# Performance work log

Measured on AMD Instinct MI355X. Metric: run time of the kernel, lower is better.

Reference implementation:

```python
import jax, jax.numpy as jnp
import numpy as np

jax.config.update("jax_enable_x64", True)  # int64 keys for lattice hashing

_EPS = float(np.finfo(np.float64).eps)
_SIGMA_SPATIAL = 5.0   # spatial stddev (voxels)
_SIGMA_COLOR = 0.25    # intensity stddev
_BASE = 8192           # per-coordinate key range
_OFF = 4096            # coordinate offset so packed keys are non-negative


def _encode(coords):
    """Pack (..., d) integer lattice coords into a single int64 key."""
    enc = jnp.zeros(coords.shape[:-1], jnp.int64)
    for i in range(coords.shape[-1]):
        enc = enc * _BASE + (coords[..., i].astype(jnp.int64) + _OFF)
    return enc


def _bilateral_features(image):
    """Bilateral features: (z,y,x)/sigma_s and intensity/sigma_c. image: (1,D,H,W)."""
    _, D, H, W = image.shape
    z, y, x = jnp.meshgrid(jnp.arange(D, dtype=jnp.float32),
                           jnp.arange(H, dtype=jnp.float32),
                           jnp.arange(W, dtype=jnp.float32), indexing="ij")
    spatial = jnp.stack([z, y, x], -1) / _SIGMA_SPATIAL            # (D,H,W,3)
    color = (image[0] / _SIGMA_COLOR)[..., None]                   # (D,H,W,1)
    return jnp.concatenate([spatial, color], -1).reshape(-1, 4)    # (N,4)


def _permutohedral(q, feats):
    """Permutohedral-lattice Gaussian filtering (splat -> blur -> slice).
    q: (N,C) float32 values, feats: (N,d) float32 positions. Returns (N,C).
    Global scale of the blur kernel cancels in the final normalization."""
    N, d = feats.shape
    dp1 = d + 1
    # ---- elevate features onto the hyperplane H_d ----
    inv_std = np.sqrt(2.0 / 3.0) * dp1
    scale = jnp.asarray([inv_std / np.sqrt((i + 1) * (i + 2)) for i in range(d)], jnp.float32)
    cf = feats * scale
    elev = [None] * dp1
    sm = jnp.zeros((N,), jnp.float32)
    for i in range(d, 0, -1):
        c = cf[:, i - 1]
        elev[i] = sm - i * c
        sm = sm + c
    elev[0] = sm
    elevated = jnp.stack(elev, axis=1)                             # (N, d+1)
    # ---- closest remainder-0 lattice point ----
    rd = jnp.round(elevated / dp1)
    rem0 = rd * dp1
    sum_rd = jnp.sum(rd, axis=1).astype(jnp.int32)
    # ---- rank of each coordinate (ties broken by index) ----
    diff = elevated - rem0
    di = diff[:, :, None]
    dj = diff[:, None, :]
    jlt = (jnp.arange(dp1)[None, :] < jnp.arange(dp1)[:, None])[None]  # mask[i,j] = j < i
    rank = jnp.sum((dj > di) | ((dj == di) & jlt), axis=2).astype(jnp.int32)
    rank = rank + sum_rd[:, None]
    low, high = rank < 0, rank > d
    rank = rank + jnp.where(low, dp1, 0) - jnp.where(high, dp1, 0)
    rem0 = rem0 + jnp.where(low, float(dp1), 0.0) - jnp.where(high, float(dp1), 0.0)
    # ---- barycentric coordinates inside the enclosing simplex ----
    v = (elevated - rem0) / dp1
    rows = jnp.arange(N)[:, None]
    bary = jnp.zeros((N, d + 2), jnp.float32)
    bary = bary.at[rows, d - rank].add(v)
    bary = bary.at[rows, dp1 - rank].add(-v)
    bary = bary.at[:, 0].add(1.0 + bary[:, dp1])
    bary = bary[:, :dp1]                                           # (N, d+1) weights per remainder
    # ---- integer keys of the d+1 simplex vertices (first d coords suffice) ----
    rem0i = rem0[:, :d].astype(jnp.int32)
    keys = jnp.stack([rem0i + jnp.where(rank[:, :d] < dp1 - r, r, r - dp1).astype(jnp.int32)
                      for r in range(dp1)], axis=1)                # (N, d+1, d)
    enc = _encode(keys).reshape(-1)
    Mpad = N * dp1
    sentinel = _BASE ** d                                          # > any real key; sorts last
    uniq, inv = jnp.unique(enc, return_inverse=True, size=Mpad, fill_value=sentinel)
    inv = inv.reshape(N, dp1)
    # ---- splat ----
    C = q.shape[1]
    vals = jnp.zeros((Mpad, C), jnp.float32).at[inv].add(bary[:, :, None] * q[:, None, :])
    # ---- blur along each of the d+1 lattice directions ----
    coords = jnp.stack([(uniq // (_BASE ** (d - 1 - i))) % _BASE - _OFF for i in range(d)],
                       axis=-1).astype(jnp.int32)                  # (Mpad, d)

    def lookup(c):
        e = _encode(c)
        pos = jnp.clip(jnp.searchsorted(uniq, e), 0, Mpad - 1)
        return pos, uniq[pos] == e

    for j in range(dp1):
        off = jnp.ones((d,), jnp.int32)
        if j < d:
            off = off.at[j].set(-d)
        p1, f1 = lookup(coords + off)
        p2, f2 = lookup(coords - off)
        n1 = jnp.where(f1[:, None], vals[p1], 0.0)
        n2 = jnp.where(f2[:, None], vals[p2], 0.0)
        vals = 0.5 * vals + 0.25 * (n1 + n2)
    # ---- slice ----
    return jnp.sum(bary[:, :, None] * vals[inv], axis=1)           # (N, C)


def setup_inputs():
    key = jax.random.key(0)
    k1, k2 = jax.random.split(key)
    input_ = jax.random.uniform(k1, (4, 96, 96, 96), dtype=jnp.float32)
    image = jax.random.uniform(k2, (1, 96, 96, 96), dtype=jnp.float32)
    return {"input_": input_, "image": image}


def reference(input_, image):
    feats = _bilateral_features(image)
    C, D, H, W = input_.shape
    q = input_.reshape(C, -1).T                                    # (N, C)
    ones = jnp.ones((q.shape[0], 1), jnp.float32)                  # fused normalization pass
    filt = _permutohedral(jnp.concatenate([q, ones], axis=1), feats)
    out = filt[:, :C] / (filt[:, C:] + _EPS)                       # == permuto(q) * 1/(permuto(1)+eps)
    return out.T.reshape(C, D, H, W)
```

## Files before the change

kernel.cpp:

```cpp
#include <hip/hip_runtime.h>
#include <hip/hip_fp16.h>
#include <stdint.h>

#define NPTS (96*96*96)
#define NP5  (NPTS*5)

#define GD1 33
#define GD2 29
#define GD3 25
#define GO0 5
#define GO1 16
#define GO2 18
#define GO3 19
#define GS3 5
#define GS2 (GD3*GS3)
#define GS1 (GD2*GS2)
#define GS0 (GD1*GS1)
#define GCELLS (31*GS0)
#define GCELLS1 (GCELLS+1)
#define GSSUM (GS0+GS1+GS2+GS3)

#define LHS 2048

struct LatPt { int cell[5]; float w[5]; };
struct V5 { float s0, s1, s2, s3, w; };


#define LATTICE_MATH(n)                                                        \
  int x = n % 96, y = (n / 96) % 96, z = n / (96 * 96);                        \
  float cf[4];                                                                 \
  cf[0] = ((float)z / 5.0f) * 2.8867513459481287f;                             \
  cf[1] = ((float)y / 5.0f) * 1.6666666666666667f;                             \
  cf[2] = ((float)x / 5.0f) * 1.1785113019775793f;                             \
  cf[3] = (imgv / 0.25f) * 0.9128709291752769f;                                \
  float elev[5];                                                               \
  float sm = 0.f;                                                              \
  _Pragma("unroll")                                                            \
  for (int i = 4; i >= 1; --i){ float c = cf[i-1]; elev[i] = sm - (float)i * c; sm += c; } \
  elev[0] = sm;                                                                \
  float rem0[5]; float sumrd_f = 0.f;                                          \
  _Pragma("unroll")                                                            \
  for (int i = 0; i < 5; i++){ float rd = rintf(elev[i] / 5.0f); rem0[i] = rd * 5.0f; sumrd_f += rd; } \
  int sum_rd = (int)sumrd_f;                                                   \
  float diff[5];                                                               \
  _Pragma("unroll")                                                            \
  for (int i = 0; i < 5; i++) diff[i] = elev[i] - rem0[i];                     \
  int rank[5];                                                                 \
  _Pragma("unroll")                                                            \
  for (int i = 0; i < 5; i++){                                                 \
    int r = 0;                                                                 \
    _Pragma("unroll")                                                          \
    for (int j = 0; j < 5; j++){                                               \
      r += (diff[j] > diff[i] || (diff[j] == diff[i] && j < i)) ? 1 : 0;       \
    }                                                                          \
    rank[i] = r + sum_rd;                                                      \
  }                                                                            \
  _Pragma("unroll")                                                            \
  for (int i = 0; i < 5; i++){                                                 \
    if (rank[i] < 0)      { rank[i] += 5; rem0[i] += 5.0f; }                   \
    else if (rank[i] > 4) { rank[i] -= 5; rem0[i] -= 5.0f; }                   \
  }                                                                            \
  float b[6] = {0.f,0.f,0.f,0.f,0.f,0.f};                                      \
  _Pragma("unroll")                                                            \
  for (int i = 0; i < 5; i++){                                                 \
    float v = (elev[i] - rem0[i]) / 5.0f;                                      \
    b[4 - rank[i]] += v;                                                       \
    b[5 - rank[i]] -= v;                                                       \
  }                                                                            \
  b[0] += 1.0f + b[5];                                                         \
  int rem0i[4];                                                                \
  _Pragma("unroll")                                                            \
  for (int i = 0; i < 4; i++) rem0i[i] = (int)rem0[i];

__device__ __forceinline__ LatPt lat_compute(int n, float imgv)
{
  LATTICE_MATH(n)
  LatPt p;
  #pragma unroll
  for (int r = 0; r < 5; r++){
    int q0 = (rem0i[0] / 5) - (rank[0] < 5 - r ? 0 : 1) + GO0;
    int q1 = (rem0i[1] / 5) - (rank[1] < 5 - r ? 0 : 1) + GO1;
    int q2 = (rem0i[2] / 5) - (rank[2] < 5 - r ? 0 : 1) + GO2;
    int q3 = (rem0i[3] / 5) - (rank[3] < 5 - r ? 0 : 1) + GO3;
    int cell = (((q0 * GD1 + q1) * GD2 + q2) * GD3 + q3) * 5 + r;
    if ((unsigned)cell >= (unsigned)GCELLS) cell = GCELLS;
    p.cell[r] = cell;
    p.w[r] = b[r];
  }
  return p;
}

__global__ void k_build_hyb(const float* __restrict__ image,
                            const float* __restrict__ input_,
                            int* __restrict__ head,
                            int4* __restrict__ nodes)
{
  __shared__ int   ls_cell[LHS];
  __shared__ int   ls_head[LHS];
  __shared__ short ls_next[1280];
  __shared__ float ls_w[1280];
  __shared__ float ls_q[256 * 4];
  __shared__ short ls_slot[1280];
  __shared__ int   ls_cnt;

  int tid = threadIdx.x;
  #pragma unroll
  for (int i = 0; i < LHS / 256; i++){
    ls_cell[tid + 256 * i] = -1;
    ls_head[tid + 256 * i] = -1;
  }
  if (tid == 0) ls_cnt = 0;
  __syncthreads();

  int n = blockIdx.x * 256 + tid;
  float q0 = input_[n], q1 = input_[NPTS + n], q2 = input_[2 * NPTS + n], q3 = input_[3 * NPTS + n];
  *reinterpret_cast<float4*>(&ls_q[tid * 4]) = make_float4(q0, q1, q2, q3);
  LatPt P = lat_compute(n, image[n]);

  #pragma unroll
  for (int r = 0; r < 5; r++){
    int cell = P.cell[r];
    unsigned int h = ((unsigned int)cell * 2654435761u) & (LHS - 1);
    while (true){
      int prev = atomicCAS(&ls_cell[h], -1, cell);
      if (prev == -1){
        int li = atomicAdd(&ls_cnt, 1);
        ls_slot[li] = (short)h;
        break;
      }
      if (prev == cell) break;
      h = (h + 1) & (LHS - 1);
    }
    int e = tid * 5 + r;
    ls_w[e] = P.w[r];
    ls_next[e] = (short)atomicExch(&ls_head[h], e);
  }
  __syncthreads();

  int cnt = ls_cnt;
  int blockBase = blockIdx.x * 1280;
  for (int i = tid; i < cnt; i += 256){
    int slot = ls_slot[i];
    int cell = ls_cell[slot];
    float s0 = 0.f, s1 = 0.f, s2 = 0.f, s3 = 0.f, s4 = 0.f;
    int e = ls_head[slot];
    while (e >= 0){
      int en = ls_next[e];
      float w = ls_w[e];
      float4 q = *reinterpret_cast<const float4*>(&ls_q[(e / 5) * 4]);
      s0 += w * q.x; s1 += w * q.y; s2 += w * q.z; s3 += w * q.w; s4 += w;
      e = en;
    }
    int node = blockBase + i;
    int old = atomicExch(&head[cell], node);
    __half2 h01 = __floats2half2_rn(s0, s1);
    __half2 h23 = __floats2half2_rn(s2, s3);
    int4 raw;
    raw.x = old;
    raw.y = *reinterpret_cast<int*>(&h01);
    raw.z = *reinterpret_cast<int*>(&h23);
    raw.w = __float_as_int(s4);
    nodes[node] = raw;
  }
}

__global__ void k_gather_agg(const int* __restrict__ head,
                             const int4* __restrict__ nodes,
                             int3* __restrict__ vals,
                             unsigned int* __restrict__ bitmap)
{
  int c = blockIdx.x * blockDim.x + threadIdx.x;
  int e = -1;
  if (c < GCELLS1) e = head[c];
  bool occ = (e >= 0);
  unsigned long long mask = __ballot(occ);
  int lane = threadIdx.x & 63;
  if (lane == 0)       bitmap[c >> 5] = (unsigned int)(mask & 0xffffffffu);
  else if (lane == 32) bitmap[c >> 5] = (unsigned int)(mask >> 32);
  if (c >= GCELLS1) return;

  float s0 = 0.f, s1 = 0.f, s2 = 0.f, s3 = 0.f, s4 = 0.f;
  while (e >= 0){
    int4 raw = nodes[e];
    __half2 h01 = *reinterpret_cast<__half2*>(&raw.y);
    __half2 h23 = *reinterpret_cast<__half2*>(&raw.z);
    float2 f01 = __half22float2(h01);
    float2 f23 = __half22float2(h23);
    s0 += f01.x; s1 += f01.y; s2 += f23.x; s3 += f23.y;
    s4 += __int_as_float(raw.w);
    e = raw.x;
  }
  __half2 o01 = __floats2half2_rn(s0, s1);
  __half2 o23 = __floats2half2_rn(s2, s3);
  int3 rec;
  rec.x = *reinterpret_cast<int*>(&o01);
  rec.y = *reinterpret_cast<int*>(&o23);
  rec.z = __float_as_int(s4);
  vals[c] = rec;
}

__device__ __forceinline__ V5 ublur(const unsigned int* __restrict__ bitmap,
                                    const int3* __restrict__ vin,
                                    int d, int dPa, int dPb, int dMa, int dMb)
{
  V5 u = {0.f, 0.f, 0.f, 0.f, 0.f};
  unsigned int wd = bitmap[d >> 5];
  if (!((wd >> (d & 31)) & 1u)) return u;
  int rd = d % 5;
  int p1 = d + (rd == 4 ? dPb : dPa);
  int p2 = d + (rd == 0 ? dMb : dMa);
  int3 a  = vin[d];
  int3 b1 = vin[p1];
  int3 b2 = vin[p2];
  float2 a01 = __half22float2(*reinterpret_cast<__half2*>(&a.x));
  float2 a23 = __half22float2(*reinterpret_cast<__half2*>(&a.y));
  float2 m01 = __half22float2(*reinterpret_cast<__half2*>(&b1.x));
  float2 m23 = __half22float2(*reinterpret_cast<__half2*>(&b1.y));
  float2 n01 = __half22float2(*reinterpret_cast<__half2*>(&b2.x));
  float2 n23 = __half22float2(*reinterpret_cast<__half2*>(&b2.y));
  u.s0 = 0.5f * a01.x + 0.25f * (m01.x + n01.x);
  u.s1 = 0.5f * a01.y + 0.25f * (m01.y + n01.y);
  u.s2 = 0.5f * a23.x + 0.25f * (m23.x + n23.x);
  u.s3 = 0.5f * a23.y + 0.25f * (m23.y + n23.y);
  u.w  = 0.5f * __int_as_float(a.z) + 0.25f * (__int_as_float(b1.z) + __int_as_float(b2.z));
  return u;
}

__global__ void k_blur2_d(const unsigned int* __restrict__ bitmap,
                          const int3* __restrict__ vin,
                          int3* __restrict__ vout,
                          int dPaA, int dPbA, int dMaA, int dMbA,
                          int dPaB, int dPbB, int dMaB, int dMbB, int zfill)
{
  int c = blockIdx.x * blockDim.x + threadIdx.x;
  if (c >= GCELLS) return;
  unsigned int w = bitmap[c >> 5];
  if (!((w >> (c & 31)) & 1u)){
    if (zfill){
      int3 zero; zero.x = 0; zero.y = 0; zero.z = 0;
      vout[c] = zero;
    }
    return;
  }
  int r = c % 5;
  int q1 = c + (r == 4 ? dPbB : dPaB);
  int q2 = c + (r == 0 ? dMbB : dMaB);

  V5 uc = ublur(bitmap, vin, c,  dPaA, dPbA, dMaA, dMbA);
  V5 u1 = ublur(bitmap, vin, q1, dPaA, dPbA, dMaA, dMbA);
  V5 u2 = ublur(bitmap, vin, q2, dPaA, dPbA, dMaA, dMbA);

  float o0 = 0.5f * uc.s0 + 0.25f * (u1.s0 + u2.s0);
  float o1 = 0.5f * uc.s1 + 0.25f * (u1.s1 + u2.s1);
  float o2 = 0.5f * uc.s2 + 0.25f * (u1.s2 + u2.s2);
  float o3 = 0.5f * uc.s3 + 0.25f * (u1.s3 + u2.s3);
  float ow = 0.5f * uc.w  + 0.25f * (u1.w  + u2.w);

  __half2 o01 = __floats2half2_rn(o0, o1);
  __half2 o23 = __floats2half2_rn(o2, o3);
  int3 rec;
  rec.x = *reinterpret_cast<int*>(&o01);
  rec.y = *reinterpret_cast<int*>(&o23);
  rec.z = __float_as_int(ow);
  vout[c] = rec;
}

__global__ void k_blur_d(const unsigned int* __restrict__ bitmap,
                         const int3* __restrict__ vin,
                         int3* __restrict__ vout,
                         int dPa, int dPb, int dMa, int dMb, int zfill)
{
  int c = blockIdx.x * blockDim.x + threadIdx.x;
  if (c >= GCELLS) return;
  unsigned int w = bitmap[c >> 5];
  if (!((w >> (c & 31)) & 1u)){
    if (zfill){
      int3 zero; zero.x = 0; zero.y = 0; zero.z = 0;
      vout[c] = zero;
    }
    return;
  }
  V5 u = ublur(bitmap, vin, c, dPa, dPb, dMa, dMb);
  __half2 o01 = __floats2half2_rn(u.s0, u.s1);
  __half2 o23 = __floats2half2_rn(u.s2, u.s3);
  int3 rec;
  rec.x = *reinterpret_cast<int*>(&o01);
  rec.y = *reinterpret_cast<int*>(&o23);
  rec.z = __float_as_int(u.w);
  vout[c] = rec;
}

__global__ void k_slice_d(const float* __restrict__ image,
                          const int3* __restrict__ vals,
                          float* __restrict__ out)
{
  int n = blockIdx.x * blockDim.x + threadIdx.x;
  if (n >= NPTS) return;
  LatPt P = lat_compute(n, image[n]);

  float s0 = 0.f, s1 = 0.f, s2 = 0.f, s3 = 0.f, s4 = 0.f;
  #pragma unroll
  for (int r = 0; r < 5; r++){
    float w = P.w[r];
    int3 rec = vals[P.cell[r]];
    float2 f01 = __half22float2(*reinterpret_cast<__half2*>(&rec.x));
    float2 f23 = __half22float2(*reinterpret_cast<__half2*>(&rec.y));
    s0 += w * f01.x; s1 += w * f01.y; s2 += w * f23.x; s3 += w * f23.y;
    s4 += w * __int_as_float(rec.z);
  }
  float denom = s4 + 2.2204460492503131e-16f;
  out[n]            = s0 / denom;
  out[NPTS + n]     = s1 / denom;
  out[2 * NPTS + n] = s2 / denom;
  out[3 * NPTS + n] = s3 / denom;
}


extern "C" void kernel_launch(void* const* d_in, const int* in_sizes, int n_in,
                              void* d_out, int out_size, void* d_ws, size_t ws_size,
                              hipStream_t stream)
{
  const float* input_ = (const float*)d_in[0];
  const float* image  = (const float*)d_in[1];
  float* out = (float*)d_out;
  char* ws = (char*)d_ws;

  const int NB = (NPTS + 255) / 256;
  const int CB = (GCELLS1 + 255) / 256;
  const size_t BMWORDS = (size_t)CB * 8;
  const int Sj[5] = { GS0, GS1, GS2, GS3, 0 };
  int dPa[5], dPb[5], dMa[5], dMb[5];
  for (int j = 0; j < 5; j++){
    dPa[j] = 1 - Sj[j];
    dPb[j] = GSSUM - Sj[j] - 4;
    dMa[j] = Sj[j] - 1;
    dMb[j] = Sj[j] - GSSUM + 4;
  }

  size_t o = 0;
  size_t off_bm   = o; o += BMWORDS * 4;              o = (o + 255) & ~(size_t)255;
  size_t off_dead = o;
  size_t off_head = o; o += (size_t)GCELLS1 * 4;      o = (o + 255) & ~(size_t)255;
  size_t off_node = o; o += (size_t)NP5 * 16;         o = (o + 255) & ~(size_t)255;
  size_t dead_end = o;
  size_t off_vA   = o; o += (size_t)GCELLS1 * 12;
  size_t vB_need  = (size_t)GCELLS1 * 12;
  size_t off_vB   = off_dead;
  if (dead_end - off_dead < vB_need || o > ws_size){
    off_vB = (o + 255) & ~(size_t)255;
  }

  unsigned int* bitmap = (unsigned int*)(ws + off_bm);
  int*          head   = (int*)(ws + off_head);
  int4*         nodes  = (int4*)(ws + off_node);
  int3*         valsA  = (int3*)(ws + off_vA);
  int3*         valsB  = (int3*)(ws + off_vB);

  hipMemsetAsync(head, 0xFF, (size_t)GCELLS1 * 4, stream);

  k_build_hyb<<<NB, 256, 0, stream>>>(image, input_, head, nodes);
  k_gather_agg<<<CB, 256, 0, stream>>>(head, nodes, valsA, bitmap);

  k_blur2_d<<<CB, 256, 0, stream>>>(bitmap, valsA, valsB,
                                    dPa[0], dPb[0], dMa[0], dMb[0],
                                    dPa[1], dPb[1], dMa[1], dMb[1], 1);
  k_blur2_d<<<CB, 256, 0, stream>>>(bitmap, valsB, valsA,
                                    dPa[2], dPb[2], dMa[2], dMb[2],
                                    dPa[3], dPb[3], dMa[3], dMb[3], 0);
  k_blur_d<<<CB, 256, 0, stream>>>(bitmap, valsA, valsB,
                                   dPa[4], dPb[4], dMa[4], dMb[4], 0);

  k_slice_d<<<NB, 256, 0, stream>>>(image, valsB, out);
}
```

Measured before the change: 176.9 us.

## Splat via float atomics into dense accumulators and drop the gather kernel

The splat no longer builds per-cell linked lists of fp16 nodes that a separate gather kernel walks. Each block's per-cell partial sums are now added directly into dense fp32 accumulators with float atomics, and the bitmap is set with atomicOr. The first blur pass reads these fp32 arrays directly, which removes the node array, the head memset and the pointer-chasing gather launch. In exchange it adds five global float atomics per cell-block pair, a larger memset of the fp32 accumulators, and nondeterministic summation order.

After: 450.3 us. 155% more time.

```diff
diff --git a/kernel.cpp b/kernel.cpp
--- a/kernel.cpp
+++ b/kernel.cpp
@@ -92,8 +92,9 @@
 
 __global__ void k_build_hyb(const float* __restrict__ image,
                             const float* __restrict__ input_,
-                            int* __restrict__ head,
-                            int4* __restrict__ nodes)
+                            float4* __restrict__ qacc,
+                            float* __restrict__ wacc,
+                            unsigned int* __restrict__ bitmap)
 {
   __shared__ int   ls_cell[LHS];
   __shared__ int   ls_head[LHS];
@@ -138,7 +139,6 @@
   __syncthreads();
 
   int cnt = ls_cnt;
-  int blockBase = blockIdx.x * 1280;
   for (int i = tid; i < cnt; i += 256){
     int slot = ls_slot[i];
     int cell = ls_cell[slot];
@@ -151,52 +151,74 @@
       s0 += w * q.x; s1 += w * q.y; s2 += w * q.z; s3 += w * q.w; s4 += w;
       e = en;
     }
-    int node = blockBase + i;
-    int old = atomicExch(&head[cell], node);
-    __half2 h01 = __floats2half2_rn(s0, s1);
-    __half2 h23 = __floats2half2_rn(s2, s3);
-    int4 raw;
-    raw.x = old;
-    raw.y = *reinterpret_cast<int*>(&h01);
-    raw.z = *reinterpret_cast<int*>(&h23);
-    raw.w = __float_as_int(s4);
-    nodes[node] = raw;
-  }
-}
-
-__global__ void k_gather_agg(const int* __restrict__ head,
-                             const int4* __restrict__ nodes,
-                             int3* __restrict__ vals,
-                             unsigned int* __restrict__ bitmap)
+    float* qc = reinterpret_cast<float*>(&qacc[cell]);
+    unsafeAtomicAdd(qc + 0, s0);
+    unsafeAtomicAdd(qc + 1, s1);
+    unsafeAtomicAdd(qc + 2, s2);
+    unsafeAtomicAdd(qc + 3, s3);
+    unsafeAtomicAdd(&wacc[cell], s4);
+    atomicOr(&bitmap[cell >> 5], 1u << (cell & 31));
+  }
+}
+
+__device__ __forceinline__ V5 ublur32(const unsigned int* __restrict__ bitmap,
+                                      const float4* __restrict__ qin,
+                                      const float* __restrict__ win,
+                                      int d, int dPa, int dPb, int dMa, int dMb)
+{
+  V5 u = {0.f, 0.f, 0.f, 0.f, 0.f};
+  unsigned int wd = bitmap[d >> 5];
+  if (!((wd >> (d & 31)) & 1u)) return u;
+  int rd = d % 5;
+  int p1 = d + (rd == 4 ? dPb : dPa);
+  int p2 = d + (rd == 0 ? dMb : dMa);
+  float4 a  = qin[d];   float aw = win[d];
+  float4 b1 = qin[p1];  float w1 = win[p1];
+  float4 b2 = qin[p2];  float w2 = win[p2];
+  u.s0 = 0.5f * a.x + 0.25f * (b1.x + b2.x);
+  u.s1 = 0.5f * a.y + 0.25f * (b1.y + b2.y);
+  u.s2 = 0.5f * a.z + 0.25f * (b1.z + b2.z);
+  u.s3 = 0.5f * a.w + 0.25f * (b1.w + b2.w);
+  u.w  = 0.5f * aw  + 0.25f * (w1 + w2);
+  return u;
+}
+
+__global__ void k_blur2_32(const unsigned int* __restrict__ bitmap,
+                           const float4* __restrict__ qin,
+                           const float* __restrict__ win,
+                           int3* __restrict__ vout,
+                           int dPaA, int dPbA, int dMaA, int dMbA,
+                           int dPaB, int dPbB, int dMaB, int dMbB)
 {
   int c = blockIdx.x * blockDim.x + threadIdx.x;
-  int e = -1;
-  if (c < GCELLS1) e = head[c];
-  bool occ = (e >= 0);
-  unsigned long long mask = __ballot(occ);
-  int lane = threadIdx.x & 63;
-  if (lane == 0)       bitmap[c >> 5] = (unsigned int)(mask & 0xffffffffu);
-  else if (lane == 32) bitmap[c >> 5] = (unsigned int)(mask >> 32);
-  if (c >= GCELLS1) return;
-
-  float s0 = 0.f, s1 = 0.f, s2 = 0.f, s3 = 0.f, s4 = 0.f;
-  while (e >= 0){
-    int4 raw = nodes[e];
-    __half2 h01 = *reinterpret_cast<__half2*>(&raw.y);
-    __half2 h23 = *reinterpret_cast<__half2*>(&raw.z);
-    float2 f01 = __half22float2(h01);
-    float2 f23 = __half22float2(h23);
-    s0 += f01.x; s1 += f01.y; s2 += f23.x; s3 += f23.y;
-    s4 += __int_as_float(raw.w);
-    e = raw.x;
-  }
-  __half2 o01 = __floats2half2_rn(s0, s1);
-  __half2 o23 = __floats2half2_rn(s2, s3);
+  if (c >= GCELLS) return;
+  unsigned int w = bitmap[c >> 5];
+  if (!((w >> (c & 31)) & 1u)){
+    int3 zero; zero.x = 0; zero.y = 0; zero.z = 0;
+    vout[c] = zero;
+    return;
+  }
+  int r = c % 5;
+  int q1 = c + (r == 4 ? dPbB : dPaB);
+  int q2 = c + (r == 0 ? dMbB : dMaB);
+
+  V5 uc = ublur32(bitmap, qin, win, c,  dPaA, dPbA, dMaA, dMbA);
+  V5 u1 = ublur32(bitmap, qin, win, q1, dPaA, dPbA, dMaA, dMbA);
+  V5 u2 = ublur32(bitmap, qin, win, q2, dPaA, dPbA, dMaA, dMbA);
+
+  float o0 = 0.5f * uc.s0 + 0.25f * (u1.s0 + u2.s0);
+  float o1 = 0.5f * uc.s1 + 0.25f * (u1.s1 + u2.s1);
+  float o2 = 0.5f * uc.s2 + 0.25f * (u1.s2 + u2.s2);
+  float o3 = 0.5f * uc.s3 + 0.25f * (u1.s3 + u2.s3);
+  float ow = 0.5f * uc.w  + 0.25f * (u1.w  + u2.w);
+
+  __half2 o01 = __floats2half2_rn(o0, o1);
+  __half2 o23 = __floats2half2_rn(o2, o3);
   int3 rec;
   rec.x = *reinterpret_cast<int*>(&o01);
   rec.y = *reinterpret_cast<int*>(&o23);
-  rec.z = __float_as_int(s4);
-  vals[c] = rec;
+  rec.z = __float_as_int(ow);
+  vout[c] = rec;
 }
 
 __device__ __forceinline__ V5 ublur(const unsigned int* __restrict__ bitmap,
@@ -338,35 +360,35 @@
   }
 
   size_t o = 0;
-  size_t off_bm   = o; o += BMWORDS * 4;              o = (o + 255) & ~(size_t)255;
+  size_t off_bm   = o; o += BMWORDS * 4;               o = (o + 255) & ~(size_t)255;
   size_t off_dead = o;
-  size_t off_head = o; o += (size_t)GCELLS1 * 4;      o = (o + 255) & ~(size_t)255;
-  size_t off_node = o; o += (size_t)NP5 * 16;         o = (o + 255) & ~(size_t)255;
+  size_t off_qa   = o; o += (size_t)GCELLS1 * 16;      o = (o + 255) & ~(size_t)255;
+  size_t off_wa   = o; o += (size_t)GCELLS1 * 4;       o = (o + 255) & ~(size_t)255;
   size_t dead_end = o;
-  size_t off_vA   = o; o += (size_t)GCELLS1 * 12;
-  size_t vB_need  = (size_t)GCELLS1 * 12;
-  size_t off_vB   = off_dead;
-  if (dead_end - off_dead < vB_need || o > ws_size){
-    off_vB = (o + 255) & ~(size_t)255;
+  size_t off_vB   = o; o += (size_t)GCELLS1 * 12;
+  size_t vA_need  = (size_t)GCELLS1 * 12;
+  size_t off_vA   = off_dead;
+  if (dead_end - off_dead < vA_need || o > ws_size){
+    off_vA = (o + 255) & ~(size_t)255;
   }
 
   unsigned int* bitmap = (unsigned int*)(ws + off_bm);
-  int*          head   = (int*)(ws + off_head);
-  int4*         nodes  = (int4*)(ws + off_node);
+  float4*       qacc   = (float4*)(ws + off_qa);
+  float*        wacc   = (float*)(ws + off_wa);
   int3*         valsA  = (int3*)(ws + off_vA);
   int3*         valsB  = (int3*)(ws + off_vB);
 
-  hipMemsetAsync(head, 0xFF, (size_t)GCELLS1 * 4, stream);
-
-  k_build_hyb<<<NB, 256, 0, stream>>>(image, input_, head, nodes);
-  k_gather_agg<<<CB, 256, 0, stream>>>(head, nodes, valsA, bitmap);
-
-  k_blur2_d<<<CB, 256, 0, stream>>>(bitmap, valsA, valsB,
-                                    dPa[0], dPb[0], dMa[0], dMb[0],
-                                    dPa[1], dPb[1], dMa[1], dMb[1], 1);
+  hipMemsetAsync(bitmap, 0, BMWORDS * 4, stream);
+  hipMemsetAsync(ws + off_qa, 0, (size_t)GCELLS1 * 20 + 256, stream);
+
+  k_build_hyb<<<NB, 256, 0, stream>>>(image, input_, qacc, wacc, bitmap);
+
+  k_blur2_32<<<CB, 256, 0, stream>>>(bitmap, qacc, wacc, valsB,
+                                     dPa[0], dPb[0], dMa[0], dMb[0],
+                                     dPa[1], dPb[1], dMa[1], dMb[1]);
   k_blur2_d<<<CB, 256, 0, stream>>>(bitmap, valsB, valsA,
                                     dPa[2], dPb[2], dMa[2], dMb[2],
-                                    dPa[3], dPb[3], dMa[3], dMb[3], 0);
+                                    dPa[3], dPb[3], dMa[3], dMb[3], 1);
   k_blur_d<<<CB, 256, 0, stream>>>(bitmap, valsA, valsB,
                                    dPa[4], dPb[4], dMa[4], dMb[4], 0);
 
```

## Fuse last three blur passes into one kernel and drop zero-fill writes

Applied to the files above, without the earlier changes.

Replaces the second two-direction blur plus the single-direction blur with one kernel that applies three blur directions by recomputing intermediate values from neighbours (27 lookups per output). Zero-filling of unoccupied cells is removed; instead, the occupancy bitmap is checked for neighbours and their values are masked to zero. The gather kernel now skips writing vals for empty cells, so unoccupied entries may hold garbage that must always be masked. This saves one launch and one full pass over the value buffer, at the cost of heavy redundant recomputation and many extra random reads.

Result: faster. 169.9 us, median of 2 (-3.9%).

```diff
diff --git a/kernel.cpp b/kernel.cpp
--- a/kernel.cpp
+++ b/kernel.cpp
@@ -177,7 +177,7 @@
   int lane = threadIdx.x & 63;
   if (lane == 0)       bitmap[c >> 5] = (unsigned int)(mask & 0xffffffffu);
   else if (lane == 32) bitmap[c >> 5] = (unsigned int)(mask >> 32);
-  if (c >= GCELLS1) return;
+  if (!occ) return;
 
   float s0 = 0.f, s1 = 0.f, s2 = 0.f, s3 = 0.f, s4 = 0.f;
   while (e >= 0){
@@ -204,14 +204,17 @@
                                     int d, int dPa, int dPb, int dMa, int dMb)
 {
   V5 u = {0.f, 0.f, 0.f, 0.f, 0.f};
-  unsigned int wd = bitmap[d >> 5];
-  if (!((wd >> (d & 31)) & 1u)) return u;
+  if (!((bitmap[d >> 5] >> (d & 31)) & 1u)) return u;
   int rd = d % 5;
   int p1 = d + (rd == 4 ? dPb : dPa);
   int p2 = d + (rd == 0 ? dMb : dMa);
+  bool o1 = (bitmap[p1 >> 5] >> (p1 & 31)) & 1u;
+  bool o2 = (bitmap[p2 >> 5] >> (p2 & 31)) & 1u;
   int3 a  = vin[d];
   int3 b1 = vin[p1];
   int3 b2 = vin[p2];
+  if (!o1){ b1.x = 0; b1.y = 0; b1.z = 0; }
+  if (!o2){ b2.x = 0; b2.y = 0; b2.z = 0; }
   float2 a01 = __half22float2(*reinterpret_cast<__half2*>(&a.x));
   float2 a23 = __half22float2(*reinterpret_cast<__half2*>(&a.y));
   float2 m01 = __half22float2(*reinterpret_cast<__half2*>(&b1.x));
@@ -226,29 +229,63 @@
   return u;
 }
 
+__device__ __forceinline__ V5 ublur2(const unsigned int* __restrict__ bitmap,
+                                     const int3* __restrict__ vin, int d,
+                                     int dPaA, int dPbA, int dMaA, int dMbA,
+                                     int dPaB, int dPbB, int dMaB, int dMbB)
+{
+  V5 o = {0.f, 0.f, 0.f, 0.f, 0.f};
+  if (!((bitmap[d >> 5] >> (d & 31)) & 1u)) return o;
+  int r = d % 5;
+  int q1 = d + (r == 4 ? dPbB : dPaB);
+  int q2 = d + (r == 0 ? dMbB : dMaB);
+  V5 uc = ublur(bitmap, vin, d,  dPaA, dPbA, dMaA, dMbA);
+  V5 u1 = ublur(bitmap, vin, q1, dPaA, dPbA, dMaA, dMbA);
+  V5 u2 = ublur(bitmap, vin, q2, dPaA, dPbA, dMaA, dMbA);
+  o.s0 = 0.5f * uc.s0 + 0.25f * (u1.s0 + u2.s0);
+  o.s1 = 0.5f * uc.s1 + 0.25f * (u1.s1 + u2.s1);
+  o.s2 = 0.5f * uc.s2 + 0.25f * (u1.s2 + u2.s2);
+  o.s3 = 0.5f * uc.s3 + 0.25f * (u1.s3 + u2.s3);
+  o.w  = 0.5f * uc.w  + 0.25f * (u1.w  + u2.w);
+  return o;
+}
+
 __global__ void k_blur2_d(const unsigned int* __restrict__ bitmap,
                           const int3* __restrict__ vin,
                           int3* __restrict__ vout,
                           int dPaA, int dPbA, int dMaA, int dMbA,
-                          int dPaB, int dPbB, int dMaB, int dMbB, int zfill)
+                          int dPaB, int dPbB, int dMaB, int dMbB)
 {
   int c = blockIdx.x * blockDim.x + threadIdx.x;
   if (c >= GCELLS) return;
-  unsigned int w = bitmap[c >> 5];
-  if (!((w >> (c & 31)) & 1u)){
-    if (zfill){
-      int3 zero; zero.x = 0; zero.y = 0; zero.z = 0;
-      vout[c] = zero;
-    }
-    return;
-  }
+  if (!((bitmap[c >> 5] >> (c & 31)) & 1u)) return;
+  V5 o = ublur2(bitmap, vin, c, dPaA, dPbA, dMaA, dMbA, dPaB, dPbB, dMaB, dMbB);
+  __half2 o01 = __floats2half2_rn(o.s0, o.s1);
+  __half2 o23 = __floats2half2_rn(o.s2, o.s3);
+  int3 rec;
+  rec.x = *reinterpret_cast<int*>(&o01);
+  rec.y = *reinterpret_cast<int*>(&o23);
+  rec.z = __float_as_int(o.w);
+  vout[c] = rec;
+}
+
+__global__ void k_blur3_d(const unsigned int* __restrict__ bitmap,
+                          const int3* __restrict__ vin,
+                          int3* __restrict__ vout,
+                          int dPaA, int dPbA, int dMaA, int dMbA,
+                          int dPaB, int dPbB, int dMaB, int dMbB,
+                          int dPaC, int dPbC, int dMaC, int dMbC)
+{
+  int c = blockIdx.x * blockDim.x + threadIdx.x;
+  if (c >= GCELLS) return;
+  if (!((bitmap[c >> 5] >> (c & 31)) & 1u)) return;
   int r = c % 5;
-  int q1 = c + (r == 4 ? dPbB : dPaB);
-  int q2 = c + (r == 0 ? dMbB : dMaB);
-
-  V5 uc = ublur(bitmap, vin, c,  dPaA, dPbA, dMaA, dMbA);
-  V5 u1 = ublur(bitmap, vin, q1, dPaA, dPbA, dMaA, dMbA);
-  V5 u2 = ublur(bitmap, vin, q2, dPaA, dPbA, dMaA, dMbA);
+  int p1 = c + (r == 4 ? dPbC : dPaC);
+  int p2 = c + (r == 0 ? dMbC : dMaC);
+
+  V5 uc = ublur2(bitmap, vin, c,  dPaA, dPbA, dMaA, dMbA, dPaB, dPbB, dMaB, dMbB);
+  V5 u1 = ublur2(bitmap, vin, p1, dPaA, dPbA, dMaA, dMbA, dPaB, dPbB, dMaB, dMbB);
+  V5 u2 = ublur2(bitmap, vin, p2, dPaA, dPbA, dMaA, dMbA, dPaB, dPbB, dMaB, dMbB);
 
   float o0 = 0.5f * uc.s0 + 0.25f * (u1.s0 + u2.s0);
   float o1 = 0.5f * uc.s1 + 0.25f * (u1.s1 + u2.s1);
@@ -262,31 +299,6 @@
   rec.x = *reinterpret_cast<int*>(&o01);
   rec.y = *reinterpret_cast<int*>(&o23);
   rec.z = __float_as_int(ow);
-  vout[c] = rec;
-}
-
-__global__ void k_blur_d(const unsigned int* __restrict__ bitmap,
-                         const int3* __restrict__ vin,
-                         int3* __restrict__ vout,
-                         int dPa, int dPb, int dMa, int dMb, int zfill)
-{
-  int c = blockIdx.x * blockDim.x + threadIdx.x;
-  if (c >= GCELLS) return;
-  unsigned int w = bitmap[c >> 5];
-  if (!((w >> (c & 31)) & 1u)){
-    if (zfill){
-      int3 zero; zero.x = 0; zero.y = 0; zero.z = 0;
-      vout[c] = zero;
-    }
-    return;
-  }
-  V5 u = ublur(bitmap, vin, c, dPa, dPb, dMa, dMb);
-  __half2 o01 = __floats2half2_rn(u.s0, u.s1);
-  __half2 o23 = __floats2half2_rn(u.s2, u.s3);
-  int3 rec;
-  rec.x = *reinterpret_cast<int*>(&o01);
-  rec.y = *reinterpret_cast<int*>(&o23);
-  rec.z = __float_as_int(u.w);
   vout[c] = rec;
 }
 
@@ -363,12 +375,11 @@
 
   k_blur2_d<<<CB, 256, 0, stream>>>(bitmap, valsA, valsB,
                                     dPa[0], dPb[0], dMa[0], dMb[0],
-                                    dPa[1], dPb[1], dMa[1], dMb[1], 1);
-  k_blur2_d<<<CB, 256, 0, stream>>>(bitmap, valsB, valsA,
+                                    dPa[1], dPb[1], dMa[1], dMb[1]);
+  k_blur3_d<<<CB, 256, 0, stream>>>(bitmap, valsB, valsA,
                                     dPa[2], dPb[2], dMa[2], dMb[2],
-                                    dPa[3], dPb[3], dMa[3], dMb[3], 0);
-  k_blur_d<<<CB, 256, 0, stream>>>(bitmap, valsA, valsB,
-                                   dPa[4], dPb[4], dMa[4], dMb[4], 0);
-
-  k_slice_d<<<NB, 256, 0, stream>>>(image, valsB, out);
-}
+                                    dPa[3], dPb[3], dMa[3], dMb[3],
+                                    dPa[4], dPb[4], dMa[4], dMb[4]);
+
+  k_slice_d<<<NB, 256, 0, stream>>>(image, valsA, out);
+}
```
